# Optimization experiments

Hardware: AMD Instinct MI355X
Metric: run time of the kernel (lower is better)

## Reference

```python
import jax, jax.numpy as jnp
import numpy as np

DIM = 512
BATCH = 1024
# row-major upper-triangle (i<j) index pairs, matching the original nested loop order
_IU, _JU = np.triu_indices(DIM, k=1)
_IU = jnp.asarray(_IU)
_JU = jnp.asarray(_JU)
FEAT_DIM = DIM + DIM * (DIM - 1) // 2 + DIM  # 131840


def setup_inputs() -> dict:
    key = jax.random.key(0)
    k1, k2, k3 = jax.random.split(key, 3)
    x = jax.random.normal(k1, (BATCH, DIM), dtype=jnp.float32)
    W = jax.random.normal(k2, (1, FEAT_DIM), dtype=jnp.float32) / np.sqrt(FEAT_DIM).astype(np.float32)
    b = jax.random.normal(k3, (1,), dtype=jnp.float32)
    return {"x": x, "W": W, "b": b}


def _quadratic_features(x):
    # pairwise products x_i * x_j for i<j in the original loop order, then squares
    pairs = x[:, _IU] * x[:, _JU]          # [B, dim*(dim-1)/2]
    squares = x * x                        # [B, dim]
    return jnp.concatenate([pairs, squares], axis=1)


def reference(x, W, b):
    feats = jnp.concatenate([x, _quadratic_features(x)], axis=1)  # [B, FEAT_DIM]
    logits = feats @ W.T + b                                      # [B, 1]
    return jax.nn.sigmoid(logits)
```

## Files before the change

kernel.cpp:

```cpp
#include <hip/hip_runtime.h>
#include <math.h>

#define DIM 512
#define BATCH 1024
#define NPAIR (DIM * (DIM - 1) / 2)
#define TPB 512

typedef short bf16x8 __attribute__((ext_vector_type(8)));
typedef float f32x4  __attribute__((ext_vector_type(4)));

__device__ __forceinline__ unsigned short f2bf(float f) {
    unsigned int u = __float_as_uint(f);
    u += 0x7fff + ((u >> 16) & 1);
    return (unsigned short)(u >> 16);
}
__device__ __forceinline__ float bf2f(unsigned short h) {
    return __uint_as_float(((unsigned int)h) << 16);
}


__global__ __launch_bounds__(TPB, 2)
void quad_gemm(const float* __restrict__ x, const float* __restrict__ W,
               float* __restrict__ partial) {
    const int bid = blockIdx.x;
    const int mg  = bid / 20;
    const int p   = bid - mg * 20;
    const int n_blk = (p < 2) ? 0 : (p < 6) ? 1 : (p < 12) ? 2 : 3;
    const int kb    = (p < 2) ? 0 : (p < 6) ? 2 : (p < 12) ? 6 : 12;
    const int kspl  = p - kb;
    const int row0 = mg * 128, n0 = n_blk * 128, k0 = kspl * 64;

    const int tid = threadIdx.x;
    const int lane = tid & 63, w = tid >> 6;
    const int wm = w >> 1, wn = w & 1;
    const int r15 = lane & 15, q = lane >> 4;

    const float* Wp  = W + DIM;
    const float* Wsq = W + DIM + NPAIR;

    __shared__ alignas(16) unsigned short sAh[128 * 64];
    __shared__ alignas(16) unsigned short sAl[128 * 64];
    __shared__ alignas(16) unsigned short sBh[128 * 64];
    __shared__ alignas(16) unsigned short sBl[128 * 64];
    __shared__ float ysum[2][128];

    #pragma unroll
    for (int u = 0; u < 2; ++u) {
        const int row = (tid >> 3) + u * 64;
        const int c   = tid & 7;
        const float* src = x + (size_t)(row0 + row) * DIM + k0 + c * 8;
        const float4 v0 = *(const float4*)(src);
        const float4 v1 = *(const float4*)(src + 4);
        const float vs[8] = {v0.x, v0.y, v0.z, v0.w, v1.x, v1.y, v1.z, v1.w};
        bf16x8 hv, lv;
        #pragma unroll
        for (int e = 0; e < 8; ++e) {
            unsigned short h = f2bf(vs[e]);
            hv[e] = (short)h;
            lv[e] = (short)f2bf(vs[e] - bf2f(h));
        }
        const int loff = row * 64 + ((c ^ (row & 7)) * 8);
        *(bf16x8*)(sAh + loff) = hv;
        *(bf16x8*)(sAl + loff) = lv;
    }

    {
        const int nr = tid & 127;
        const int n  = n0 + nr;
        const int cb = (tid >> 7) * 2;
        #pragma unroll
        for (int u = 0; u < 2; ++u) {
            const int c = cb + u;
            float vs[8];
            int k  = k0 + c * 8;
            int ro = k * (DIM - 2) - (k * (k - 1)) / 2 - 1;
            #pragma unroll
            for (int e = 0; e < 8; ++e) {
                const float wv = Wp[ro + n];
                vs[e] = (n > k) ? wv : ((n == k) ? Wsq[k] : 0.f);
                ro += DIM - 2 - k;
                ++k;
            }
            bf16x8 hv, lv;
            #pragma unroll
            for (int e = 0; e < 8; ++e) {
                unsigned short h = f2bf(vs[e]);
                hv[e] = (short)h;
                lv[e] = (short)f2bf(vs[e] - bf2f(h));
            }
            const int loff = nr * 64 + ((c ^ (nr & 7)) * 8);
            *(bf16x8*)(sBh + loff) = hv;
            *(bf16x8*)(sBl + loff) = lv;
        }
    }

    float xv[4][2][4];
    float wlv[4];
    #pragma unroll
    for (int sn = 0; sn < 4; ++sn) {
        const int n = n0 + wn * 64 + sn * 16 + r15;
        wlv[sn] = (kspl == 0) ? W[n] : 0.f;
        #pragma unroll
        for (int sm = 0; sm < 2; ++sm) {
            const int mbase = row0 + wm * 32 + sm * 16 + q * 4;
            #pragma unroll
            for (int r = 0; r < 4; ++r)
                xv[sn][sm][r] = x[(size_t)(mbase + r) * DIM + n];
        }
    }
    __syncthreads();

    f32x4 acc[2][4];
    #pragma unroll
    for (int i = 0; i < 2; ++i)
        #pragma unroll
        for (int j = 0; j < 4; ++j) acc[i][j] = (f32x4){0.f, 0.f, 0.f, 0.f};

    #pragma unroll
    for (int ks = 0; ks < 2; ++ks) {
        const int c = ks * 4 + q;
        bf16x8 ah[2], al[2];
        #pragma unroll
        for (int sm = 0; sm < 2; ++sm) {
            const int row = wm * 32 + sm * 16 + r15;
            const int off = row * 64 + ((c ^ (row & 7)) * 8);
            ah[sm] = *(const bf16x8*)(sAh + off);
            al[sm] = *(const bf16x8*)(sAl + off);
        }
        #pragma unroll
        for (int sn = 0; sn < 4; ++sn) {
            const int row = wn * 64 + sn * 16 + r15;
            const int off = row * 64 + ((c ^ (row & 7)) * 8);
            const bf16x8 bh = *(const bf16x8*)(sBh + off);
            const bf16x8 bl = *(const bf16x8*)(sBl + off);
            acc[0][sn] = __builtin_amdgcn_mfma_f32_16x16x32_bf16(ah[0], bh, acc[0][sn], 0, 0, 0);
            acc[1][sn] = __builtin_amdgcn_mfma_f32_16x16x32_bf16(ah[1], bh, acc[1][sn], 0, 0, 0);
            acc[0][sn] = __builtin_amdgcn_mfma_f32_16x16x32_bf16(al[0], bh, acc[0][sn], 0, 0, 0);
            acc[1][sn] = __builtin_amdgcn_mfma_f32_16x16x32_bf16(al[1], bh, acc[1][sn], 0, 0, 0);
            acc[0][sn] = __builtin_amdgcn_mfma_f32_16x16x32_bf16(ah[0], bl, acc[0][sn], 0, 0, 0);
            acc[1][sn] = __builtin_amdgcn_mfma_f32_16x16x32_bf16(ah[1], bl, acc[1][sn], 0, 0, 0);
        }
    }

    float yl[2][4];
    #pragma unroll
    for (int sm = 0; sm < 2; ++sm)
        #pragma unroll
        for (int r = 0; r < 4; ++r) yl[sm][r] = 0.f;

    #pragma unroll
    for (int sn = 0; sn < 4; ++sn)
        #pragma unroll
        for (int sm = 0; sm < 2; ++sm)
            #pragma unroll
            for (int r = 0; r < 4; ++r)
                yl[sm][r] += (acc[sm][sn][r] + wlv[sn]) * xv[sn][sm][r];

    #pragma unroll
    for (int off = 1; off < 16; off <<= 1) {
        #pragma unroll
        for (int sm = 0; sm < 2; ++sm)
            #pragma unroll
            for (int r = 0; r < 4; ++r)
                yl[sm][r] += __shfl_xor(yl[sm][r], off);
    }
    if (r15 == 0) {
        #pragma unroll
        for (int sm = 0; sm < 2; ++sm)
            #pragma unroll
            for (int r = 0; r < 4; ++r)
                ysum[wn][wm * 32 + sm * 16 + q * 4 + r] = yl[sm][r];
    }
    __syncthreads();
    if (tid < 128) {
        const float z = ysum[0][tid] + ysum[1][tid];
        partial[(size_t)p * BATCH + row0 + tid] = z;
    }
}

__global__ __launch_bounds__(64)
void finalize(const float* __restrict__ partial, const float* __restrict__ bias,
              float* __restrict__ out) {
    const int t = blockIdx.x * 64 + threadIdx.x;
    float v[20];
    #pragma unroll
    for (int s = 0; s < 20; ++s) v[s] = partial[(size_t)s * BATCH + t];
    float z = (((v[0] + v[1]) + (v[2] + v[3])) + ((v[4] + v[5]) + (v[6] + v[7]))) +
              (((v[8] + v[9]) + (v[10] + v[11])) + ((v[12] + v[13]) + (v[14] + v[15]))) +
              ((v[16] + v[17]) + (v[18] + v[19])) + bias[0];
    out[t] = 1.0f / (1.0f + expf(-z));
}

extern "C" void kernel_launch(void* const* d_in, const int* in_sizes, int n_in,
                              void* d_out, int out_size, void* d_ws, size_t ws_size,
                              hipStream_t stream) {
    const float* x = (const float*)d_in[0];
    const float* W = (const float*)d_in[1];
    const float* b = (const float*)d_in[2];
    float* out = (float*)d_out;

    float* partial = (float*)d_ws;

    hipLaunchKernelGGL(quad_gemm, dim3(160), dim3(TPB), 0, stream, x, W, partial);
    hipLaunchKernelGGL(finalize,  dim3(BATCH / 64), dim3(64), 0, stream, partial, b, out);
}
```

Measured before the change: 12.81 us.

## Precompute bf16 split operands in a prep kernel and fuse finalize via last-block counter

A new prep kernel converts x and the upper-triangular W matrix into hi/lo bf16 arrays in workspace once. The GEMM blocks then just copy the pre-split tiles into shared memory instead of gathering W with strided loads and converting per block. The separate finalize kernel is removed: each block stores its partial, bumps a per-row-group atomic counter, and the last block sums the partials and applies the sigmoid. The cost is an extra kernel launch and a global round trip for the converted data, plus relaxed-atomic ordering that relies on an explicit vmcnt wait.

```diff
diff --git a/kernel.cpp b/kernel.cpp
--- a/kernel.cpp
+++ b/kernel.cpp
@@ -18,10 +18,70 @@
     return __uint_as_float(((unsigned int)h) << 16);
 }
 
+#define UTL_OFF 262144
+#define XH_OFF  524288
+#define XL_OFF  1048576
+#define PART_BYTE 3145728u
+#define CNT_BYTE  (3145728u + 81920u)
+
+
+__global__ __launch_bounds__(256)
+void prep(const float* __restrict__ x, const float* __restrict__ W,
+          unsigned short* __restrict__ Uth, unsigned short* __restrict__ Utl,
+          unsigned short* __restrict__ Xh, unsigned short* __restrict__ Xl,
+          int* __restrict__ cnt) {
+    const int bid = blockIdx.x, tid = threadIdx.x;
+    if (bid == 0 && tid < 8) cnt[tid] = 0;
+    if (bid < 256) {
+        const int gid = bid * 256 + tid;
+        const float4 v0 = ((const float4*)x)[(size_t)gid * 2];
+        const float4 v1 = ((const float4*)x)[(size_t)gid * 2 + 1];
+        const float vs[8] = {v0.x, v0.y, v0.z, v0.w, v1.x, v1.y, v1.z, v1.w};
+        bf16x8 hv, lv;
+        #pragma unroll
+        for (int e = 0; e < 8; ++e) {
+            unsigned short h = f2bf(vs[e]);
+            hv[e] = (short)h;
+            lv[e] = (short)f2bf(vs[e] - bf2f(h));
+        }
+        ((bf16x8*)Xh)[gid] = hv;
+        ((bf16x8*)Xl)[gid] = lv;
+    } else {
+        const int u  = (bid - 256) * 256 + tid;
+        const int n  = u & 511;
+        const int kc = u >> 9;
+        const int k0 = kc * 8;
+        const float* Wp  = W + DIM;
+        const float* Wsq = W + DIM + NPAIR;
+        float vs[8];
+        int k  = k0;
+        int ro = k0 * (DIM - 2) - (k0 * (k0 - 1)) / 2 - 1;
+        #pragma unroll
+        for (int e = 0; e < 8; ++e) {
+            const float wv = Wp[ro + n];
+            vs[e] = (n > k) ? wv : ((n == k) ? Wsq[k] : 0.f);
+            ro += DIM - 2 - k;
+            ++k;
+        }
+        bf16x8 hv, lv;
+        #pragma unroll
+        for (int e = 0; e < 8; ++e) {
+            unsigned short h = f2bf(vs[e]);
+            hv[e] = (short)h;
+            lv[e] = (short)f2bf(vs[e] - bf2f(h));
+        }
+        *(bf16x8*)(Uth + (size_t)n * DIM + k0) = hv;
+        *(bf16x8*)(Utl + (size_t)n * DIM + k0) = lv;
+    }
+}
 
 __global__ __launch_bounds__(TPB, 2)
 void quad_gemm(const float* __restrict__ x, const float* __restrict__ W,
-               float* __restrict__ partial) {
+               const unsigned short* __restrict__ Uth, const unsigned short* __restrict__ Utl,
+               const unsigned short* __restrict__ Xh, const unsigned short* __restrict__ Xl,
+               const float* __restrict__ bias,
+               float* __restrict__ partial, int* __restrict__ cnt,
+               float* __restrict__ out) {
     const int bid = blockIdx.x;
     const int mg  = bid / 20;
     const int p   = bid - mg * 20;
@@ -35,63 +95,30 @@
     const int wm = w >> 1, wn = w & 1;
     const int r15 = lane & 15, q = lane >> 4;
 
-    const float* Wp  = W + DIM;
-    const float* Wsq = W + DIM + NPAIR;
-
     __shared__ alignas(16) unsigned short sAh[128 * 64];
     __shared__ alignas(16) unsigned short sAl[128 * 64];
     __shared__ alignas(16) unsigned short sBh[128 * 64];
     __shared__ alignas(16) unsigned short sBl[128 * 64];
     __shared__ float ysum[2][128];
-
-    #pragma unroll
-    for (int u = 0; u < 2; ++u) {
-        const int row = (tid >> 3) + u * 64;
-        const int c   = tid & 7;
-        const float* src = x + (size_t)(row0 + row) * DIM + k0 + c * 8;
-        const float4 v0 = *(const float4*)(src);
-        const float4 v1 = *(const float4*)(src + 4);
-        const float vs[8] = {v0.x, v0.y, v0.z, v0.w, v1.x, v1.y, v1.z, v1.w};
-        bf16x8 hv, lv;
-        #pragma unroll
-        for (int e = 0; e < 8; ++e) {
-            unsigned short h = f2bf(vs[e]);
-            hv[e] = (short)h;
-            lv[e] = (short)f2bf(vs[e] - bf2f(h));
-        }
+    __shared__ int lastFlag;
+
+    #pragma unroll
+    for (int s = 0; s < 2; ++s) {
+        const int slot = tid + s * TPB;
+        const int row = slot >> 3, c = slot & 7;
+        const int g    = (row0 + row) * DIM + k0 + c * 8;
         const int loff = row * 64 + ((c ^ (row & 7)) * 8);
-        *(bf16x8*)(sAh + loff) = hv;
-        *(bf16x8*)(sAl + loff) = lv;
-    }
-
-    {
-        const int nr = tid & 127;
-        const int n  = n0 + nr;
-        const int cb = (tid >> 7) * 2;
-        #pragma unroll
-        for (int u = 0; u < 2; ++u) {
-            const int c = cb + u;
-            float vs[8];
-            int k  = k0 + c * 8;
-            int ro = k * (DIM - 2) - (k * (k - 1)) / 2 - 1;
-            #pragma unroll
-            for (int e = 0; e < 8; ++e) {
-                const float wv = Wp[ro + n];
-                vs[e] = (n > k) ? wv : ((n == k) ? Wsq[k] : 0.f);
-                ro += DIM - 2 - k;
-                ++k;
-            }
-            bf16x8 hv, lv;
-            #pragma unroll
-            for (int e = 0; e < 8; ++e) {
-                unsigned short h = f2bf(vs[e]);
-                hv[e] = (short)h;
-                lv[e] = (short)f2bf(vs[e] - bf2f(h));
-            }
-            const int loff = nr * 64 + ((c ^ (nr & 7)) * 8);
-            *(bf16x8*)(sBh + loff) = hv;
-            *(bf16x8*)(sBl + loff) = lv;
-        }
+        *(bf16x8*)(sAh + loff) = *(const bf16x8*)(Xh + g);
+        *(bf16x8*)(sAl + loff) = *(const bf16x8*)(Xl + g);
+    }
+    #pragma unroll
+    for (int s = 0; s < 2; ++s) {
+        const int slot = tid + s * TPB;
+        const int row = slot >> 3, c = slot & 7;
+        const int g    = (n0 + row) * DIM + k0 + c * 8;
+        const int loff = row * 64 + ((c ^ (row & 7)) * 8);
+        *(bf16x8*)(sBh + loff) = *(const bf16x8*)(Uth + g);
+        *(bf16x8*)(sBl + loff) = *(const bf16x8*)(Utl + g);
     }
 
     float xv[4][2][4];
@@ -172,23 +199,29 @@
                 ysum[wn][wm * 32 + sm * 16 + q * 4 + r] = yl[sm][r];
     }
     __syncthreads();
+
     if (tid < 128) {
         const float z = ysum[0][tid] + ysum[1][tid];
-        partial[(size_t)p * BATCH + row0 + tid] = z;
-    }
-}
-
-__global__ __launch_bounds__(64)
-void finalize(const float* __restrict__ partial, const float* __restrict__ bias,
-              float* __restrict__ out) {
-    const int t = blockIdx.x * 64 + threadIdx.x;
-    float v[20];
-    #pragma unroll
-    for (int s = 0; s < 20; ++s) v[s] = partial[(size_t)s * BATCH + t];
-    float z = (((v[0] + v[1]) + (v[2] + v[3])) + ((v[4] + v[5]) + (v[6] + v[7]))) +
-              (((v[8] + v[9]) + (v[10] + v[11])) + ((v[12] + v[13]) + (v[14] + v[15]))) +
-              ((v[16] + v[17]) + (v[18] + v[19])) + bias[0];
-    out[t] = 1.0f / (1.0f + expf(-z));
+        __hip_atomic_store(&partial[(size_t)p * BATCH + row0 + tid], z,
+                           __ATOMIC_RELAXED, __HIP_MEMORY_SCOPE_AGENT);
+    }
+    asm volatile("s_waitcnt vmcnt(0)" ::: "memory");
+    __syncthreads();
+    if (tid == 0) {
+        const int old = __hip_atomic_fetch_add(&cnt[mg], 1,
+                                               __ATOMIC_RELAXED, __HIP_MEMORY_SCOPE_AGENT);
+        lastFlag = (old == 19);
+    }
+    __syncthreads();
+
+    if (lastFlag && tid < 128) {
+        float z = bias[0];
+        #pragma unroll
+        for (int s = 0; s < 20; ++s)
+            z += __hip_atomic_load(&partial[(size_t)s * BATCH + row0 + tid],
+                                   __ATOMIC_RELAXED, __HIP_MEMORY_SCOPE_AGENT);
+        out[row0 + tid] = 1.0f / (1.0f + expf(-z));
+    }
 }
 
 extern "C" void kernel_launch(void* const* d_in, const int* in_sizes, int n_in,
@@ -199,8 +232,15 @@
     const float* b = (const float*)d_in[2];
     float* out = (float*)d_out;
 
-    float* partial = (float*)d_ws;
-
-    hipLaunchKernelGGL(quad_gemm, dim3(160), dim3(TPB), 0, stream, x, W, partial);
-    hipLaunchKernelGGL(finalize,  dim3(BATCH / 64), dim3(64), 0, stream, partial, b, out);
-}
+    unsigned short* us = (unsigned short*)d_ws;
+    unsigned short* Uth = us;
+    unsigned short* Utl = us + UTL_OFF;
+    unsigned short* Xh  = us + XH_OFF;
+    unsigned short* Xl  = us + XL_OFF;
+    float* partial = (float*)((char*)d_ws + PART_BYTE);
+    int*   cnt     = (int*)((char*)d_ws + CNT_BYTE);
+
+    hipLaunchKernelGGL(prep,      dim3(384), dim3(256), 0, stream, x, W, Uth, Utl, Xh, Xl, cnt);
+    hipLaunchKernelGGL(quad_gemm, dim3(160), dim3(TPB), 0, stream, x, W, Uth, Utl, Xh, Xl,
+                       b, partial, cnt, out);
+}
```

Result: slower. 18.20 us (+42.1%).
